# Kernel tuning notes

Hardware: AMD Instinct MI355X
Metric: run time of the kernel (lower is better)

Reference implementation:

```python
import jax, jax.numpy as jnp
import numpy as np

NUM_SLOTS = 3
NUM_ORIENTS = 8
PATCH_SIZE = 81  # 9x9 board
BUY_SIZE = NUM_SLOTS * NUM_ORIENTS * PATCH_SIZE  # 1944
ACTIONS = 1 + PATCH_SIZE + BUY_SIZE  # 2026
NEG = -1.0e9
EPS = 1e-5

B = 4096
C_IN = 256
HID = 256


def setup_inputs() -> dict:
    key = jax.random.key(0)
    ks = jax.random.split(key, 12)
    s = 0.05
    return {
        "x": jax.random.normal(ks[0], (B, C_IN, 9, 9), jnp.float32),
        "action_mask": jax.random.randint(ks[1], (B, ACTIONS), 0, 2, dtype=jnp.int32),
        # p_conv: 1x1 conv, no bias (use_batch_norm=True) -> weight (HID, C_IN)
        "conv_w": jax.random.normal(ks[2], (HID, C_IN), jnp.float32) * s,
        # BatchNorm2d (inference form with running stats)
        "bn_gamma": jnp.ones((HID,), jnp.float32),
        "bn_beta": jnp.zeros((HID,), jnp.float32),
        "bn_mean": jax.random.normal(ks[3], (HID,), jnp.float32) * 0.1,
        "bn_var": jax.random.uniform(ks[4], (HID,), jnp.float32, 0.5, 1.5),
        "type_w": jax.random.normal(ks[5], (3, HID), jnp.float32) * s,
        "type_b": jnp.zeros((3,), jnp.float32),
        "patch_w": jax.random.normal(ks[6], (1, HID), jnp.float32) * s,
        "patch_b": jnp.zeros((1,), jnp.float32),
        "slot_w": jax.random.normal(ks[7], (NUM_SLOTS, HID), jnp.float32) * s,
        "slot_b": jnp.zeros((NUM_SLOTS,), jnp.float32),
        "orient_w": jax.random.normal(ks[8], (NUM_SLOTS * NUM_ORIENTS, HID), jnp.float32) * s,
        "orient_b": jnp.zeros((NUM_SLOTS * NUM_ORIENTS,), jnp.float32),
        "pos_w": jax.random.normal(ks[9], (NUM_SLOTS * NUM_ORIENTS, HID), jnp.float32) * s,
        "pos_b": jnp.zeros((NUM_SLOTS * NUM_ORIENTS,), jnp.float32),
    }


def _masked_logsoftmax(logits, mask_bool):
    lg = jnp.where(mask_bool, logits, NEG)
    return jnp.maximum(jax.nn.log_softmax(lg, axis=-1), -100.0)


def reference(x, action_mask, conv_w, bn_gamma, bn_beta, bn_mean, bn_var,
              type_w, type_b, patch_w, patch_b, slot_w, slot_b,
              orient_w, orient_b, pos_w, pos_b):
    b = x.shape[0]
    # 1x1 conv + BN (eval) + ReLU
    p = jnp.einsum('bchw,oc->bohw', x, conv_w)
    scale = bn_gamma * jax.lax.rsqrt(bn_var + EPS)
    p = jax.nn.relu(p * scale[None, :, None, None] + (bn_beta - bn_mean * scale)[None, :, None, None])
    p_mean = p.mean(axis=(2, 3))  # (B, HID)

    # masks from action_mask layout [pass | 81 patch | 1944 buy]
    am = action_mask > 0
    patch_mask = am[:, 1:1 + PATCH_SIZE]
    buy4d = am[:, 82:82 + BUY_SIZE].reshape(b, NUM_SLOTS, NUM_ORIENTS, PATCH_SIZE)
    type_mask = jnp.stack([am[:, 0], patch_mask.any(-1), buy4d.reshape(b, -1).any(-1)], axis=-1)
    orient_mask = buy4d.any(-1)
    slot_mask = orient_mask.any(-1)

    type_lp = _masked_logsoftmax(p_mean @ type_w.T + type_b, type_mask)          # (B,3)
    patch_logits = jnp.einsum('bchw,oc->bohw', p, patch_w).reshape(b, PATCH_SIZE) \
        + patch_b[0]
    patch_lp = _masked_logsoftmax(patch_logits, patch_mask)                       # (B,81)
    slot_lp = _masked_logsoftmax(p_mean @ slot_w.T + slot_b, slot_mask)           # (B,3)
    orient_lp = _masked_logsoftmax(
        (p_mean @ orient_w.T + orient_b).reshape(b, NUM_SLOTS, NUM_ORIENTS), orient_mask)
    pos_logits = (jnp.einsum('bchw,oc->bohw', p, pos_w) + pos_b[None, :, None, None]) \
        .reshape(b, NUM_SLOTS, NUM_ORIENTS, PATCH_SIZE)
    pos_lp = _masked_logsoftmax(pos_logits, buy4d)                                # (B,3,8,81)

    pass_lp = type_lp[:, 0:1]
    patch_joint = type_lp[:, 1:2] + patch_lp
    buy_joint = (type_lp[:, 2:3, None, None] + slot_lp[:, :, None, None]
                 + orient_lp[:, :, :, None] + pos_lp).reshape(b, BUY_SIZE)
    return jnp.concatenate([pass_lp, patch_joint, buy_joint], axis=1)  # (B, 2026)
```

## Files before the change

### kernel.cpp

```cpp
#include <hip/hip_runtime.h>

#define ACT 2026
#define NEGV -1.0e9f

typedef short short8 __attribute__((ext_vector_type(8)));
typedef float f32x4 __attribute__((ext_vector_type(4)));

__device__ __forceinline__ unsigned f2bf(float f) {
  unsigned u = __float_as_uint(f);
  return (u + 0x7FFFu + ((u >> 16) & 1u)) >> 16;
}

__device__ __forceinline__ unsigned cvtpk(float lo, float hi) {
  unsigned r;
  asm("v_cvt_pk_bf16_f32 %0, %1, %2" : "=v"(r) : "v"(lo), "v"(hi));
  return r;
}

#define GL16(gp, lp) __builtin_amdgcn_global_load_lds(                         \
    (const __attribute__((address_space(1))) void*)(gp),                       \
    (__attribute__((address_space(3))) void*)(lp), 16, 0, 0)

__global__ void prep_w_kernel(const float* __restrict__ conv_w,
                              const float* __restrict__ pos_w,
                              const float* __restrict__ patch_w,
                              unsigned short* __restrict__ wimg,
                              unsigned short* __restrict__ w2img) {
  int g = blockIdx.x * 256 + threadIdx.x;
  if (g < 8192) {
    int r = g & 15, gq = (g >> 4) & 3, mtg = (g >> 6) & 15, ks = g >> 10;
    const float* src = conv_w + (mtg * 16 + r) * 256 + ks * 32 + gq * 8;
    unsigned v0 = f2bf(src[0]) | (f2bf(src[1]) << 16);
    unsigned v1 = f2bf(src[2]) | (f2bf(src[3]) << 16);
    unsigned v2 = f2bf(src[4]) | (f2bf(src[5]) << 16);
    unsigned v3 = f2bf(src[6]) | (f2bf(src[7]) << 16);
    uint4 q; q.x = v0; q.y = v1; q.z = v2; q.w = v3;
    *(uint4*)(wimg + g * 8) = q;
  } else if (g < 9216) {
    int g2 = g - 8192;
    int r = g2 & 15, gq = (g2 >> 4) & 3, mt = (g2 >> 6) & 1, ks2 = g2 >> 7;
    int m2 = mt * 16 + r;
    int o0 = ks2 * 32 + gq * 8;
    unsigned short v[8];
#pragma unroll
    for (int e = 0; e < 8; ++e) {
      float f = 0.f;
      if (m2 < 24) f = pos_w[m2 * 256 + o0 + e];
      else if (m2 == 24) f = patch_w[o0 + e];
      v[e] = (unsigned short)f2bf(f);
    }
    uint4 q;
    q.x = (unsigned)v[0] | ((unsigned)v[1] << 16);
    q.y = (unsigned)v[2] | ((unsigned)v[3] << 16);
    q.z = (unsigned)v[4] | ((unsigned)v[5] << 16);
    q.w = (unsigned)v[6] | ((unsigned)v[7] << 16);
    *(uint4*)(w2img + g2 * 8) = q;
  }
}

__global__ __launch_bounds__(256, 3)
void policy_main(const float* __restrict__ x,
                 const int* __restrict__ am,
                 const unsigned short* __restrict__ wimg,
                 const unsigned short* __restrict__ w2img,
                 const float* __restrict__ bn_gamma, const float* __restrict__ bn_beta,
                 const float* __restrict__ bn_mean, const float* __restrict__ bn_var,
                 const float* __restrict__ type_w, const float* __restrict__ type_b,
                 const float* __restrict__ patch_b,
                 const float* __restrict__ slot_w, const float* __restrict__ slot_b,
                 const float* __restrict__ orient_w, const float* __restrict__ orient_b,
                 const float* __restrict__ pos_b,
                 float* __restrict__ out)
{
  __shared__ __align__(16) char s_big[49152];
  __shared__ __align__(16) float s_scale[256];
  __shared__ __align__(16) float s_bias[256];
  __shared__ __align__(16) float s_pmean[256];
  __shared__ float s_part[240];
  __shared__ float s_hl[30];
  __shared__ float s_tlp[3], s_slp[3], s_olp[24];
  __shared__ int s_omask[24];
  __shared__ int s_misc[6];

  char* f32buf = s_big;
  char* bfimg  = s_big + 31104;
  unsigned short* pT = (unsigned short*)s_big;
  float* s_out2 = (float*)s_big;

  const int tid = threadIdx.x;
  const int w  = tid >> 6;
  const int l  = tid & 63;
  const int b  = blockIdx.x;
  const float* xb = x + (size_t)b * (256 * 81);

  {
    float sc = bn_gamma[tid] * rsqrtf(bn_var[tid] + 1e-5f);
    s_scale[tid] = sc;
    s_bias[tid]  = bn_beta[tid] - bn_mean[tid] * sc;
  }

  const int kg = l >> 4;
  const int kr = l & 15;
  const int g4 = kg * 4;

  f32x4 acc[4][6];
#pragma unroll
  for (int i = 0; i < 4; ++i)
#pragma unroll
    for (int j = 0; j < 6; ++j) {
      f32x4 z = {0.f, 0.f, 0.f, 0.f};
      acc[i][j] = z;
    }

  auto STAGE = [&](int ks) {
    const char* g = (const char*)xb + ks * 10368;
    char* lb = f32buf + (ks % 3) * 10368;
    int o1 = w * 162;
    int o2 = o1 + 64;
    int o3 = (w == 3) ? 584 : o1 + 128;
    GL16(g + (o1 + l) * 16, lb + o1 * 16);
    GL16(g + (o2 + l) * 16, lb + o2 * 16);
    GL16(g + (o3 + l) * 16, lb + o3 * 16);
  };

  auto TRANSPOSE = [&](int t) {
    const float* src = (const float*)(f32buf + (t % 3) * 10368);
    char* dst = bfimg + (t & 1) * 6144;
    {
      int q = tid;
      int nt_ = q >> 6, kr_ = (q >> 2) & 15, kg_ = q & 3;
      const float* s = src + kg_ * 648 + nt_ * 16 + kr_;
      uint4 v;
      v.x = cvtpk(s[0],   s[81]);
      v.y = cvtpk(s[162], s[243]);
      v.z = cvtpk(s[324], s[405]);
      v.w = cvtpk(s[486], s[567]);
      *(uint4*)(dst + q * 16) = v;
    }
    if (tid < 128) {
      int q = 256 + tid;
      int nt_ = q >> 6, kr_ = (q >> 2) & 15, kg_ = q & 3;
      const float* s = src + kg_ * 648 + nt_ * 16 + kr_;
      uint4 v;
      v.x = cvtpk(s[0],   s[81]);
      v.y = cvtpk(s[162], s[243]);
      v.z = cvtpk(s[324], s[405]);
      v.w = cvtpk(s[486], s[567]);
      *(uint4*)(dst + q * 16) = v;
    }
  };

  STAGE(0); STAGE(1); STAGE(2);
  asm volatile("s_waitcnt vmcnt(6)" ::: "memory");
  __builtin_amdgcn_s_barrier();
  __builtin_amdgcn_sched_barrier(0);
  TRANSPOSE(0);
  asm volatile("s_waitcnt vmcnt(3)" ::: "memory");
  asm volatile("s_waitcnt lgkmcnt(0)" ::: "memory");
  __builtin_amdgcn_s_barrier();
  __builtin_amdgcn_sched_barrier(0);

  const int fragoff = (kr * 4 + kg) * 16;

  auto STEP = [&](int k) {
    short8 af[4];
    {
      const unsigned short* ab = wimg + k * 8192 + w * 2048 + kg * 128 + kr * 8;
      af[0] = *(const short8*)(ab);
      af[1] = *(const short8*)(ab + 512);
      af[2] = *(const short8*)(ab + 1024);
      af[3] = *(const short8*)(ab + 1536);
    }
    __builtin_amdgcn_sched_barrier(0);
    if (k + 3 < 8) STAGE(k + 3);
    if (k + 1 < 8) TRANSPOSE(k + 1);
    const char* bi = bfimg + (k & 1) * 6144;
#pragma unroll
    for (int nt = 0; nt < 6; ++nt) {
      short8 bf = *(const short8*)(bi + nt * 1024 + fragoff);
      acc[0][nt] = __builtin_amdgcn_mfma_f32_16x16x32_bf16(af[0], bf, acc[0][nt], 0, 0, 0);
      acc[1][nt] = __builtin_amdgcn_mfma_f32_16x16x32_bf16(af[1], bf, acc[1][nt], 0, 0, 0);
      acc[2][nt] = __builtin_amdgcn_mfma_f32_16x16x32_bf16(af[2], bf, acc[2][nt], 0, 0, 0);
      acc[3][nt] = __builtin_amdgcn_mfma_f32_16x16x32_bf16(af[3], bf, acc[3][nt], 0, 0, 0);
    }
    if (k < 7) {
      if (k + 3 < 8) asm volatile("s_waitcnt vmcnt(3)" ::: "memory");
      else           asm volatile("s_waitcnt vmcnt(0)" ::: "memory");
      asm volatile("s_waitcnt lgkmcnt(0)" ::: "memory");
      __builtin_amdgcn_s_barrier();
      __builtin_amdgcn_sched_barrier(0);
    } else {
      __syncthreads();
    }
  };

  STEP(0); STEP(1); STEP(2); STEP(3);
  STEP(4); STEP(5); STEP(6); STEP(7);

#pragma unroll
  for (int mi = 0; mi < 4; ++mi) {
    int ob = w * 64 + mi * 16 + g4;
    float sc0 = s_scale[ob], sc1 = s_scale[ob + 1], sc2 = s_scale[ob + 2], sc3 = s_scale[ob + 3];
    float bi0 = s_bias[ob],  bi1 = s_bias[ob + 1],  bi2 = s_bias[ob + 2],  bi3 = s_bias[ob + 3];
    float vs0 = 0.f, vs1 = 0.f, vs2 = 0.f, vs3 = 0.f;
    int ks2 = ob >> 5;
    int j2  = (ob >> 3) & 3;
    int e0  = ob & 7;
    char* pbase = (char*)pT + ks2 * 6144 + j2 * 256 + kr * 16 + e0 * 2;
#pragma unroll
    for (int nt = 0; nt < 6; ++nt) {
      float v0 = fmaxf(acc[mi][nt][0] * sc0 + bi0, 0.f);
      float v1 = fmaxf(acc[mi][nt][1] * sc1 + bi1, 0.f);
      float v2 = fmaxf(acc[mi][nt][2] * sc2 + bi2, 0.f);
      float v3 = fmaxf(acc[mi][nt][3] * sc3 + bi3, 0.f);
      if (nt < 5 || kr == 0) { vs0 += v0; vs1 += v1; vs2 += v2; vs3 += v3; }
      uint2 pvv;
      pvv.x = cvtpk(v0, v1);
      pvv.y = cvtpk(v2, v3);
      *(uint2*)(pbase + nt * 1024) = pvv;
    }
    float vv[4] = {vs0, vs1, vs2, vs3};
#pragma unroll
    for (int i = 0; i < 4; ++i) {
      float s = vv[i];
      s += __shfl_xor(s, 1);
      s += __shfl_xor(s, 2);
      s += __shfl_xor(s, 4);
      s += __shfl_xor(s, 8);
      vv[i] = s;
    }
    if (kr == 0) {
      s_pmean[ob]     = vv[0] * (1.f / 81.f);
      s_pmean[ob + 1] = vv[1] * (1.f / 81.f);
      s_pmean[ob + 2] = vv[2] * (1.f / 81.f);
      s_pmean[ob + 3] = vv[3] * (1.f / 81.f);
    }
  }

  const int* amr = am + (size_t)b * ACT;
  for (int t = w; t < 25; t += 4) {
    int off = (t < 24) ? (82 + t * 81) : 1;
    int v1 = amr[off + l];
    int v2 = (l < 17) ? amr[off + 64 + l] : 0;
    unsigned long long bal = __ballot((v1 | v2) != 0);
    if (l == 0) {
      int any = (bal != 0ULL) ? 1 : 0;
      if (t < 24) s_omask[t] = any; else s_misc[0] = any;
    }
  }
  __syncthreads();

  {
    const int mt  = w & 1;
    const int ntb = (w >> 1) * 3;
    f32x4 acc2[3];
#pragma unroll
    for (int t = 0; t < 3; ++t) { f32x4 z = {0.f, 0.f, 0.f, 0.f}; acc2[t] = z; }
#pragma unroll
    for (int ks2 = 0; ks2 < 8; ++ks2) {
      const unsigned short* ap = w2img + ((ks2 * 2 + mt) * 4 + kg) * 128 + kr * 8;
      short8 a2 = *(const short8*)ap;
#pragma unroll
      for (int t = 0; t < 3; ++t) {
        const short8* bp = (const short8*)((const char*)pT + ks2 * 6144 + (ntb + t) * 1024 + kg * 256 + kr * 16);
        acc2[t] = __builtin_amdgcn_mfma_f32_16x16x32_bf16(a2, *bp, acc2[t], 0, 0, 0);
      }
    }
    __syncthreads();
#pragma unroll
    for (int t = 0; t < 3; ++t) {
      int hw = (ntb + t) * 16 + kr;
      int m2 = mt * 16 + g4;
#pragma unroll
      for (int i = 0; i < 4; ++i)
        s_out2[(m2 + i) * 104 + hw] = acc2[t][i];
    }
  }

  if (tid < 240) {
    int h = tid >> 3, seg = tid & 7;
    const float* wp = (h < 3) ? (type_w + h * 256)
                    : (h < 6) ? (slot_w + (h - 3) * 256)
                              : (orient_w + (h - 6) * 256);
    float p = 0.f;
    int base = seg * 32;
#pragma unroll 8
    for (int e = 0; e < 32; ++e) p += s_pmean[base + e] * wp[base + e];
    s_part[tid] = p;
  }
  __syncthreads();

  if (tid < 30) {
    float a = 0.f;
#pragma unroll
    for (int e = 0; e < 8; ++e) a += s_part[tid * 8 + e];
    a += (tid < 3) ? type_b[tid] : (tid < 6) ? slot_b[tid - 3] : orient_b[tid - 6];
    s_hl[tid] = a;
  }
  if (tid == 32) {
    int sa0 = 0, sa1 = 0, sa2 = 0;
#pragma unroll
    for (int r = 0; r < 8; ++r) { sa0 |= s_omask[r]; sa1 |= s_omask[8 + r]; sa2 |= s_omask[16 + r]; }
    s_misc[1] = sa0; s_misc[2] = sa1; s_misc[3] = sa2;
    s_misc[4] = sa0 | sa1 | sa2;
  }
  __syncthreads();

  if (tid == 0) {
    int mk0 = amr[0] > 0, mk1 = s_misc[0], mk2 = s_misc[4];
    float g0 = mk0 ? s_hl[0] : NEGV;
    float g1 = mk1 ? s_hl[1] : NEGV;
    float g2 = mk2 ? s_hl[2] : NEGV;
    float m = fmaxf(fmaxf(g0, g1), g2);
    float sum = __expf(g0 - m) + __expf(g1 - m) + __expf(g2 - m);
    float ls = m + __logf(sum);
    s_tlp[0] = fmaxf(g0 - ls, -100.f);
    s_tlp[1] = fmaxf(g1 - ls, -100.f);
    s_tlp[2] = fmaxf(g2 - ls, -100.f);
  } else if (tid == 1) {
    float g[3]; float m = -3.0e38f;
#pragma unroll
    for (int s = 0; s < 3; ++s) { g[s] = s_misc[1 + s] ? s_hl[3 + s] : NEGV; m = fmaxf(m, g[s]); }
    float sum = 0.f;
#pragma unroll
    for (int s = 0; s < 3; ++s) sum += __expf(g[s] - m);
    float ls = m + __logf(sum);
#pragma unroll
    for (int s = 0; s < 3; ++s) s_slp[s] = fmaxf(g[s] - ls, -100.f);
  } else if (tid >= 2 && tid < 5) {
    int s = tid - 2;
    float g[8]; float m = -3.0e38f;
#pragma unroll
    for (int r = 0; r < 8; ++r) { g[r] = s_omask[s * 8 + r] ? s_hl[6 + s * 8 + r] : NEGV; m = fmaxf(m, g[r]); }
    float sum = 0.f;
#pragma unroll
    for (int r = 0; r < 8; ++r) sum += __expf(g[r] - m);
    float ls = m + __logf(sum);
#pragma unroll
    for (int r = 0; r < 8; ++r) s_olp[s * 8 + r] = fmaxf(g[r] - ls, -100.f);
  }
  __syncthreads();

  float* ob_out = out + (size_t)b * ACT;
  for (int t = w; t < 25; t += 4) {
    int off = (t < 24) ? (82 + t * 81) : 1;
    float badd = (t < 24) ? pos_b[t] : patch_b[0];
    int a1 = amr[off + l];
    int a2v = (l < 17) ? amr[off + 64 + l] : 0;
    float lg1 = (a1 > 0) ? (s_out2[t * 104 + l] + badd) : NEGV;
    float lg2 = (l < 17 && a2v > 0) ? (s_out2[t * 104 + 64 + l] + badd) : NEGV;
    float mx = fmaxf(lg1, (l < 17) ? lg2 : -3.0e38f);
#pragma unroll
    for (int mm = 1; mm < 64; mm <<= 1) mx = fmaxf(mx, __shfl_xor(mx, mm));
    float sm = __expf(lg1 - mx) + ((l < 17) ? __expf(lg2 - mx) : 0.f);
#pragma unroll
    for (int mm = 1; mm < 64; mm <<= 1) sm += __shfl_xor(sm, mm);
    float lse = mx + __logf(sm);
    float lp1 = fmaxf(lg1 - lse, -100.f);
    float lp2 = fmaxf(lg2 - lse, -100.f);
    float addj; int obase;
    if (t < 24) { addj = s_tlp[2] + s_slp[t >> 3] + s_olp[t]; obase = 82 + t * 81; }
    else        { addj = s_tlp[1];                             obase = 1; }
    ob_out[obase + l] = addj + lp1;
    if (l < 17) ob_out[obase + 64 + l] = addj + lp2;
    if (t == 24 && l == 0) ob_out[0] = s_tlp[0];
  }
}

extern "C" void kernel_launch(void* const* d_in, const int* in_sizes, int n_in,
                              void* d_out, int out_size, void* d_ws, size_t ws_size,
                              hipStream_t stream) {
  (void)in_sizes; (void)n_in; (void)out_size; (void)ws_size;
  const float* x        = (const float*)d_in[0];
  const int*   amask    = (const int*)d_in[1];
  const float* conv_w   = (const float*)d_in[2];
  const float* bn_gamma = (const float*)d_in[3];
  const float* bn_beta  = (const float*)d_in[4];
  const float* bn_mean  = (const float*)d_in[5];
  const float* bn_var   = (const float*)d_in[6];
  const float* type_w   = (const float*)d_in[7];
  const float* type_b   = (const float*)d_in[8];
  const float* patch_w  = (const float*)d_in[9];
  const float* patch_b  = (const float*)d_in[10];
  const float* slot_w   = (const float*)d_in[11];
  const float* slot_b   = (const float*)d_in[12];
  const float* orient_w = (const float*)d_in[13];
  const float* orient_b = (const float*)d_in[14];
  const float* pos_w    = (const float*)d_in[15];
  const float* pos_b    = (const float*)d_in[16];
  float* outp = (float*)d_out;

  unsigned short* wimg  = (unsigned short*)d_ws;
  unsigned short* w2img = wimg + 65536;

  prep_w_kernel<<<36, 256, 0, stream>>>(conv_w, pos_w, patch_w, wimg, w2img);
  policy_main<<<4096, 256, 0, stream>>>(x, amask, wimg, w2img,
                                        bn_gamma, bn_beta, bn_mean, bn_var,
                                        type_w, type_b, patch_b,
                                        slot_w, slot_b, orient_w, orient_b,
                                        pos_b, outp);
}
```

Measured before the change: 200.0 us.

## Double block to 512 threads, split GEMM rows across 8 waves and overlap head work

Each block now runs 8 waves instead of 4. The conv GEMM's output rows are split so each wave holds half the accumulators, and staging and transpose work is spread across more threads. In the second phase, waves 0-3 do the pos/patch MFMA while waves 4-7 compute the action-mask reductions and the head dot products at the same time. This aims for more latency hiding and lower register pressure per wave, at the cost of extra barriers and a higher LDS/occupancy constraint per block.

Result: faster. 194.9 us (-2.6%).

```diff
diff --git a/kernel.cpp b/kernel.cpp
--- a/kernel.cpp
+++ b/kernel.cpp
@@ -58,7 +58,7 @@
   }
 }
 
-__global__ __launch_bounds__(256, 3)
+__global__ __launch_bounds__(512, 4)
 void policy_main(const float* __restrict__ x,
                  const int* __restrict__ am,
                  const unsigned short* __restrict__ wimg,
@@ -93,7 +93,7 @@
   const int b  = blockIdx.x;
   const float* xb = x + (size_t)b * (256 * 81);
 
-  {
+  if (tid < 256) {
     float sc = bn_gamma[tid] * rsqrtf(bn_var[tid] + 1e-5f);
     s_scale[tid] = sc;
     s_bias[tid]  = bn_beta[tid] - bn_mean[tid] * sc;
@@ -103,9 +103,9 @@
   const int kr = l & 15;
   const int g4 = kg * 4;
 
-  f32x4 acc[4][6];
-#pragma unroll
-  for (int i = 0; i < 4; ++i)
+  f32x4 acc[2][6];
+#pragma unroll
+  for (int i = 0; i < 2; ++i)
 #pragma unroll
     for (int j = 0; j < 6; ++j) {
       f32x4 z = {0.f, 0.f, 0.f, 0.f};
@@ -115,18 +115,16 @@
   auto STAGE = [&](int ks) {
     const char* g = (const char*)xb + ks * 10368;
     char* lb = f32buf + (ks % 3) * 10368;
-    int o1 = w * 162;
-    int o2 = o1 + 64;
-    int o3 = (w == 3) ? 584 : o1 + 128;
+    int o1 = w * 81;
+    int o2 = o1 + 17;
     GL16(g + (o1 + l) * 16, lb + o1 * 16);
     GL16(g + (o2 + l) * 16, lb + o2 * 16);
-    GL16(g + (o3 + l) * 16, lb + o3 * 16);
   };
 
   auto TRANSPOSE = [&](int t) {
     const float* src = (const float*)(f32buf + (t % 3) * 10368);
     char* dst = bfimg + (t & 1) * 6144;
-    {
+    if (tid < 384) {
       int q = tid;
       int nt_ = q >> 6, kr_ = (q >> 2) & 15, kg_ = q & 3;
       const float* s = src + kg_ * 648 + nt_ * 16 + kr_;
@@ -137,25 +135,14 @@
       v.w = cvtpk(s[486], s[567]);
       *(uint4*)(dst + q * 16) = v;
     }
-    if (tid < 128) {
-      int q = 256 + tid;
-      int nt_ = q >> 6, kr_ = (q >> 2) & 15, kg_ = q & 3;
-      const float* s = src + kg_ * 648 + nt_ * 16 + kr_;
-      uint4 v;
-      v.x = cvtpk(s[0],   s[81]);
-      v.y = cvtpk(s[162], s[243]);
-      v.z = cvtpk(s[324], s[405]);
-      v.w = cvtpk(s[486], s[567]);
-      *(uint4*)(dst + q * 16) = v;
-    }
   };
 
   STAGE(0); STAGE(1); STAGE(2);
-  asm volatile("s_waitcnt vmcnt(6)" ::: "memory");
+  asm volatile("s_waitcnt vmcnt(4)" ::: "memory");
   __builtin_amdgcn_s_barrier();
   __builtin_amdgcn_sched_barrier(0);
   TRANSPOSE(0);
-  asm volatile("s_waitcnt vmcnt(3)" ::: "memory");
+  asm volatile("s_waitcnt vmcnt(2)" ::: "memory");
   asm volatile("s_waitcnt lgkmcnt(0)" ::: "memory");
   __builtin_amdgcn_s_barrier();
   __builtin_amdgcn_sched_barrier(0);
@@ -163,13 +150,11 @@
   const int fragoff = (kr * 4 + kg) * 16;
 
   auto STEP = [&](int k) {
-    short8 af[4];
+    short8 af[2];
     {
-      const unsigned short* ab = wimg + k * 8192 + w * 2048 + kg * 128 + kr * 8;
+      const unsigned short* ab = wimg + k * 8192 + w * 1024 + kg * 128 + kr * 8;
       af[0] = *(const short8*)(ab);
       af[1] = *(const short8*)(ab + 512);
-      af[2] = *(const short8*)(ab + 1024);
-      af[3] = *(const short8*)(ab + 1536);
     }
     __builtin_amdgcn_sched_barrier(0);
     if (k + 3 < 8) STAGE(k + 3);
@@ -180,11 +165,9 @@
       short8 bf = *(const short8*)(bi + nt * 1024 + fragoff);
       acc[0][nt] = __builtin_amdgcn_mfma_f32_16x16x32_bf16(af[0], bf, acc[0][nt], 0, 0, 0);
       acc[1][nt] = __builtin_amdgcn_mfma_f32_16x16x32_bf16(af[1], bf, acc[1][nt], 0, 0, 0);
-      acc[2][nt] = __builtin_amdgcn_mfma_f32_16x16x32_bf16(af[2], bf, acc[2][nt], 0, 0, 0);
-      acc[3][nt] = __builtin_amdgcn_mfma_f32_16x16x32_bf16(af[3], bf, acc[3][nt], 0, 0, 0);
     }
     if (k < 7) {
-      if (k + 3 < 8) asm volatile("s_waitcnt vmcnt(3)" ::: "memory");
+      if (k + 3 < 8) asm volatile("s_waitcnt vmcnt(2)" ::: "memory");
       else           asm volatile("s_waitcnt vmcnt(0)" ::: "memory");
       asm volatile("s_waitcnt lgkmcnt(0)" ::: "memory");
       __builtin_amdgcn_s_barrier();
@@ -198,8 +181,8 @@
   STEP(4); STEP(5); STEP(6); STEP(7);
 
 #pragma unroll
-  for (int mi = 0; mi < 4; ++mi) {
-    int ob = w * 64 + mi * 16 + g4;
+  for (int mi = 0; mi < 2; ++mi) {
+    int ob = w * 32 + mi * 16 + g4;
     float sc0 = s_scale[ob], sc1 = s_scale[ob + 1], sc2 = s_scale[ob + 2], sc3 = s_scale[ob + 3];
     float bi0 = s_bias[ob],  bi1 = s_bias[ob + 1],  bi2 = s_bias[ob + 2],  bi3 = s_bias[ob + 3];
     float vs0 = 0.f, vs1 = 0.f, vs2 = 0.f, vs3 = 0.f;
@@ -236,26 +219,16 @@
       s_pmean[ob + 3] = vv[3] * (1.f / 81.f);
     }
   }
+  __syncthreads();
 
   const int* amr = am + (size_t)b * ACT;
-  for (int t = w; t < 25; t += 4) {
-    int off = (t < 24) ? (82 + t * 81) : 1;
-    int v1 = amr[off + l];
-    int v2 = (l < 17) ? amr[off + 64 + l] : 0;
-    unsigned long long bal = __ballot((v1 | v2) != 0);
-    if (l == 0) {
-      int any = (bal != 0ULL) ? 1 : 0;
-      if (t < 24) s_omask[t] = any; else s_misc[0] = any;
-    }
-  }
-  __syncthreads();
-
-  {
-    const int mt  = w & 1;
-    const int ntb = (w >> 1) * 3;
-    f32x4 acc2[3];
-#pragma unroll
-    for (int t = 0; t < 3; ++t) { f32x4 z = {0.f, 0.f, 0.f, 0.f}; acc2[t] = z; }
+  const int mt  = w & 1;
+  const int ntb = (w >> 1) * 3;
+  f32x4 acc2[3];
+#pragma unroll
+  for (int t = 0; t < 3; ++t) { f32x4 z = {0.f, 0.f, 0.f, 0.f}; acc2[t] = z; }
+
+  if (w < 4) {
 #pragma unroll
     for (int ks2 = 0; ks2 < 8; ++ks2) {
       const unsigned short* ap = w2img + ((ks2 * 2 + mt) * 4 + kg) * 128 + kr * 8;
@@ -266,7 +239,33 @@
         acc2[t] = __builtin_amdgcn_mfma_f32_16x16x32_bf16(a2, *bp, acc2[t], 0, 0, 0);
       }
     }
-    __syncthreads();
+  } else {
+    for (int t = w - 4; t < 25; t += 4) {
+      int off = (t < 24) ? (82 + t * 81) : 1;
+      int v1 = amr[off + l];
+      int v2 = (l < 17) ? amr[off + 64 + l] : 0;
+      unsigned long long bal = __ballot((v1 | v2) != 0);
+      if (l == 0) {
+        int any = (bal != 0ULL) ? 1 : 0;
+        if (t < 24) s_omask[t] = any; else s_misc[0] = any;
+      }
+    }
+    int hh = tid - 256;
+    if (hh < 240) {
+      int h = hh >> 3, seg = hh & 7;
+      const float* wp = (h < 3) ? (type_w + h * 256)
+                      : (h < 6) ? (slot_w + (h - 3) * 256)
+                                : (orient_w + (h - 6) * 256);
+      float p = 0.f;
+      int base = seg * 32;
+#pragma unroll 8
+      for (int e = 0; e < 32; ++e) p += s_pmean[base + e] * wp[base + e];
+      s_part[hh] = p;
+    }
+  }
+  __syncthreads();
+
+  if (w < 4) {
 #pragma unroll
     for (int t = 0; t < 3; ++t) {
       int hw = (ntb + t) * 16 + kr;
@@ -276,20 +275,6 @@
         s_out2[(m2 + i) * 104 + hw] = acc2[t][i];
     }
   }
-
-  if (tid < 240) {
-    int h = tid >> 3, seg = tid & 7;
-    const float* wp = (h < 3) ? (type_w + h * 256)
-                    : (h < 6) ? (slot_w + (h - 3) * 256)
-                              : (orient_w + (h - 6) * 256);
-    float p = 0.f;
-    int base = seg * 32;
-#pragma unroll 8
-    for (int e = 0; e < 32; ++e) p += s_pmean[base + e] * wp[base + e];
-    s_part[tid] = p;
-  }
-  __syncthreads();
-
   if (tid < 30) {
     float a = 0.f;
 #pragma unroll
@@ -342,7 +327,7 @@
   __syncthreads();
 
   float* ob_out = out + (size_t)b * ACT;
-  for (int t = w; t < 25; t += 4) {
+  for (int t = w; t < 25; t += 8) {
     int off = (t < 24) ? (82 + t * 81) : 1;
     float badd = (t < 24) ? pos_b[t] : patch_b[0];
     int a1 = amr[off + l];
@@ -394,7 +379,7 @@
   unsigned short* w2img = wimg + 65536;
 
   prep_w_kernel<<<36, 256, 0, stream>>>(conv_w, pos_w, patch_w, wimg, w2img);
-  policy_main<<<4096, 256, 0, stream>>>(x, amask, wimg, w2img,
+  policy_main<<<4096, 512, 0, stream>>>(x, amask, wimg, w2img,
                                         bn_gamma, bn_beta, bn_mean, bn_var,
                                         type_w, type_b, patch_b,
                                         slot_w, slot_b, orient_w, orient_b,
```
